# Kernel tuning notes

Hardware: AMD Instinct MI355X
Metric: run time of the kernel (lower is better)

The kernel has to match this reference:

```python
import jax, jax.numpy as jnp
import numpy as np

B, F, T, H, K = 512, 64, 64, 512, 4  # batch, in_feat, timesteps, hidden, num cells (air0,bed0,air1,bed1)


def setup_inputs() -> dict:
    key = jax.random.key(0)
    ks = jax.random.split(key, 10)
    s = 1.0 / np.sqrt(H)
    u = lambda k, shape: jax.random.uniform(k, shape, jnp.float32, -s, s)
    return {
        "data": jax.random.normal(ks[0], (B, F, T), jnp.float32),
        "init": jax.random.normal(ks[1], (B, H), jnp.float32),
        # stacked params for the 4 branches in order [air0, bed0, air1, bed1]
        "fc_in_W": u(ks[2], (K, H, F)),
        "fc_in_b": u(ks[3], (K, H)),
        "Wih": u(ks[4], (K, 3 * H, H)),   # torch GRUCell weight_ih, gate order r,z,n
        "Whh": u(ks[5], (K, 3 * H, H)),
        "bih": u(ks[6], (K, 3 * H)),
        "bhh": u(ks[7], (K, 3 * H)),
        "fc_out_W": u(ks[8], (2, H)),     # [air, bed] output heads (Linear(512,1))
        "fc_out_b": u(ks[9], (2,)),
    }


def reference(data, init, fc_in_W, fc_in_b, Wih, Whh, bih, bhh, fc_out_W, fc_out_b):
    # Input projections (Linear + ReLU; Dropout is identity in eval): [T, K, B, H]
    proj = jax.nn.relu(jnp.einsum('bft,kof->tkbo', data, fc_in_W) + fc_in_b[None, :, None, :])
    # branches 2,3 (air1, bed1) consume the sequence reversed (data[:, :, 63-i])
    x_seq = jnp.concatenate([proj[:, :2], proj[::-1, 2:]], axis=1)  # [T, K, B, H]

    h0 = jnp.broadcast_to(init[None], (K,) + init.shape)  # all 4 cells start from init

    def step(h, x):  # h, x: [K, B, H]
        gi = jnp.einsum('kbi,koi->kbo', x, Wih) + bih[:, None, :]
        gh = jnp.einsum('kbi,koi->kbo', h, Whh) + bhh[:, None, :]
        ir, iz, inn = jnp.split(gi, 3, axis=-1)
        hr, hz, hn = jnp.split(gh, 3, axis=-1)
        r = jax.nn.sigmoid(ir + hr)
        z = jax.nn.sigmoid(iz + hz)
        n = jnp.tanh(inn + r * hn)
        h_new = (1.0 - z) * n + z * h
        return h_new, h_new

    _, hs = jax.lax.scan(step, h0, x_seq)  # [T, K, B, H]

    # output i (1..64) combines fwd hidden[i] with bwd hidden[65-i] -> reverse bwd stack
    air = hs[:, 0] + hs[::-1, 2]  # [T, B, H]
    bed = hs[:, 1] + hs[::-1, 3]
    air_out = (jnp.einsum('tbh,h->tb', air, fc_out_W[0]) + fc_out_b[0]).T  # [B, T]
    bed_out = (jnp.einsum('tbh,h->tb', bed, fc_out_W[1]) + fc_out_b[1]).T
    return air_out, bed_out
```

## Files before the change

kernel.cpp:

```cpp
#include <hip/hip_runtime.h>
#include <hip/hip_bf16.h>

typedef __hip_bfloat16 bf16;
typedef __attribute__((ext_vector_type(8))) short short8;
typedef __attribute__((ext_vector_type(4))) float f32x4;

#define Hdim 512
#define Bdim 512
#define Tdim 64
#define Fdim 64
#define NC   4

__device__ __forceinline__ float sigmoidf_(float x){ return 1.f/(1.f + __expf(-x)); }
__device__ __forceinline__ float tanhf_(float x){
  float t = __expf(-2.f*fabsf(x));
  float r = (1.f - t)/(1.f + t);
  return copysignf(r, x);
}
__device__ __forceinline__ float bf2f_(short u){
  return __uint_as_float(((unsigned)(unsigned short)u) << 16);
}
__device__ __forceinline__ short f2bf_(float f){
  bf16 b = (bf16)f;
  return *(short*)&b;
}

__global__ __launch_bounds__(256) void pack_kernel(const float* __restrict__ src,
                                                   bf16* __restrict__ dst, int n){
  int idx = (blockIdx.x*256 + threadIdx.x)*4;
  if (idx < n){
    float4 v = *(const float4*)(src + idx);
    dst[idx+0] = (bf16)v.x;
    dst[idx+1] = (bf16)v.y;
    dst[idx+2] = (bf16)v.z;
    dst[idx+3] = (bf16)v.w;
  }
}

__global__ __launch_bounds__(256) void transpose_kernel(const float* __restrict__ data,
                                                        bf16* __restrict__ dataT){
  __shared__ bf16 tile[64*65];
  int b = blockIdx.x;
  int tid = threadIdx.x;
  for (int i = 0; i < 16; ++i){
    int idx = tid + i*256;
    int f = idx >> 6, t = idx & 63;
    tile[f*65 + t] = (bf16)data[(b*64 + f)*64 + t];
  }
  __syncthreads();
  for (int i = 0; i < 16; ++i){
    int idx = tid + i*256;
    int t = idx >> 6, f = idx & 63;
    dataT[(t*Bdim + b)*64 + f] = tile[f*65 + t];
  }
}

__global__ __launch_bounds__(256) void init_kernel(const float* __restrict__ init_h,
                            bf16* __restrict__ h_b1, unsigned* __restrict__ flags){
  int idx = blockIdx.x*256 + threadIdx.x;
  int k = idx >> 18;
  int rem = idx & 262143;
  int bg = rem >> 9;
  int o  = rem & 511;
  int dst = ((k*2 + (bg >> 8))*16 + (o >> 5))*8192 + (bg & 255)*32 + (o & 31);
  h_b1[dst] = (bf16)init_h[rem];
  if (idx < 512) flags[idx] = 0u;
}

__global__ __launch_bounds__(256) void proj_kernel(const bf16* __restrict__ dataT,
    const bf16* __restrict__ fc_in_W, const float* __restrict__ fc_in_b,
    bf16* __restrict__ x_seq){
  __shared__ short ldsA[64*72];
  __shared__ short ldsW[128*72];
  int blk = blockIdx.x;
  int s  = blk >> 7;
  int k  = (blk >> 5) & 3;
  int bt = (blk >> 2) & 7;
  int on = blk & 3;
  int tid = threadIdx.x;
  int lane = tid & 63, wid = tid >> 6;
  int quad = lane >> 4, l16 = lane & 15;
  int src_t = (k < 2) ? s : (Tdim - 1 - s);

  const short* Ag = (const short*)(dataT + (src_t*Bdim + bt*64)*Fdim);
  #pragma unroll
  for (int i = 0; i < 2; ++i){
    int c = tid + i*256; int r = c >> 3, off = c & 7;
    *(int4*)(&ldsA[r*72 + off*8]) = *(const int4*)(&Ag[r*64 + off*8]);
  }
  const short* Wg = (const short*)(fc_in_W + (k*Hdim + on*128)*Fdim);
  #pragma unroll
  for (int i = 0; i < 4; ++i){
    int c = tid + i*256; int r = c >> 3, off = c & 7;
    *(int4*)(&ldsW[r*72 + off*8]) = *(const int4*)(&Wg[r*64 + off*8]);
  }
  __syncthreads();

  f32x4 acc[2][4];
  #pragma unroll
  for (int nt=0; nt<2; ++nt)
    #pragma unroll
    for (int rb=0; rb<4; ++rb) acc[nt][rb] = (f32x4){0.f,0.f,0.f,0.f};

  #pragma unroll
  for (int kk = 0; kk < 2; ++kk){
    int io = kk*32 + quad*8;
    short8 a[4];
    #pragma unroll
    for (int rb=0; rb<4; ++rb) a[rb] = *(const short8*)(&ldsA[(rb*16+l16)*72 + io]);
    #pragma unroll
    for (int nt=0; nt<2; ++nt){
      short8 bw = *(const short8*)(&ldsW[(wid*32 + nt*16 + l16)*72 + io]);
      #pragma unroll
      for (int rb=0; rb<4; ++rb)
        acc[nt][rb] = __builtin_amdgcn_mfma_f32_16x16x32_bf16(a[rb], bw, acc[nt][rb], 0,0,0);
    }
  }

  #pragma unroll
  for (int nt=0; nt<2; ++nt){
    int o = on*128 + wid*32 + nt*16 + l16;
    float bias = fc_in_b[k*Hdim + o];
    #pragma unroll
    for (int rb=0; rb<4; ++rb){
      #pragma unroll
      for (int reg=0; reg<4; ++reg){
        int b = bt*64 + rb*16 + quad*4 + reg;
        float v = acc[nt][rb][reg] + bias;
        v = v > 0.f ? v : 0.f;
        x_seq[((size_t)(s*NC + k)*Bdim + b)*Hdim + o] = (bf16)v;
      }
    }
  }
}

__global__ __launch_bounds__(512) void rnn_kernel(
    const bf16* __restrict__ x_seq, const float* __restrict__ init_h,
    bf16* __restrict__ h_b0, bf16* __restrict__ h_b1,
    const float* __restrict__ Wih, const float* __restrict__ Whh,
    const float* __restrict__ bih, const float* __restrict__ bhh,
    const float* __restrict__ fc_out_W,
    bf16* __restrict__ gi, float* __restrict__ part,
    unsigned* __restrict__ flags, unsigned* __restrict__ xslot)
{
  __shared__ short wlds[3*2*16*512];
  __shared__ int sslot;

  int tid = threadIdx.x;
  int lane = tid & 63, wid = tid >> 6;
  int quad = lane >> 4, l16 = lane & 15;

  unsigned xcc;
  asm volatile("s_getreg_b32 %0, hwreg(HW_REG_XCC_ID)" : "=s"(xcc));
  xcc &= 7u;
  if (tid == 0)
    sslot = (int)__hip_atomic_fetch_add(&xslot[xcc*32], 1u,
                __ATOMIC_RELAXED, __HIP_MEMORY_SCOPE_WORKGROUP);
  __syncthreads();
  int grp = (int)xcc;
  int k   = grp >> 1;
  int bt  = grp & 1;
  int slot = sslot & 31;
  int producer = (slot < 16);
  int j    = slot & 15;
  int obase = j*32;
  int rot  = j;
  unsigned* gflags = flags + grp*32;

  const float* Wsrc = producer ? Wih : Whh;
  for (int i = tid; i < 3*2*16*64; i += 512){
    int plane = i >> 11;
    int rem   = i & 2047;
    int nt    = rem >> 10;
    int rem2  = rem & 1023;
    int kc    = rem2 >> 6;
    int ln    = rem2 & 63;
    int ll16  = ln & 15, lq = ln >> 4;
    const float* srcp = Wsrc +
        ((size_t)(k*3 + plane)*Hdim + obase + nt*16 + ll16)*Hdim + kc*32 + lq*8;
    float4 f0 = *(const float4*)srcp;
    float4 f1 = *(const float4*)(srcp + 4);
    short8 pk;
    pk[0]=f2bf_(f0.x); pk[1]=f2bf_(f0.y); pk[2]=f2bf_(f0.z); pk[3]=f2bf_(f0.w);
    pk[4]=f2bf_(f1.x); pk[5]=f2bf_(f1.y); pk[6]=f2bf_(f1.z); pk[7]=f2bf_(f1.w);
    *(int4*)(&wlds[i*8]) = *(int4*)&pk;
  }

  #define GEMM32X(ABASE) do {                                                   \
    const short* ap0_ = (ABASE) + (wid*32 + l16)*Hdim + quad*8;                 \
    const short* ap1_ = ap0_ + 16*Hdim;                                         \
    short8 ab_[4][2];                                                           \
    _Pragma("unroll")                                                           \
    for (int d=0; d<4; ++d){                                                    \
      int c_ = (d + rot) & 15;                                                  \
      ab_[d][0] = *(const short8*)(ap0_ + c_*32);                               \
      ab_[d][1] = *(const short8*)(ap1_ + c_*32);                               \
    }                                                                           \
    short8 bb_[2][6];                                                           \
    _Pragma("unroll")                                                           \
    for (int p=0; p<6; ++p)                                                     \
      bb_[0][p] = *(const short8*)(&wlds[((p*16 + rot)<<9) + (lane<<3)]);       \
    _Pragma("unroll")                                                           \
    for (int kc=0; kc<16; ++kc){                                                \
      short8 a0_ = ab_[kc&3][0], a1_ = ab_[kc&3][1];                            \
      if (kc < 12){                                                             \
        int c_ = (kc + 4 + rot) & 15;                                           \
        ab_[kc&3][0] = *(const short8*)(ap0_ + c_*32);                          \
        ab_[kc&3][1] = *(const short8*)(ap1_ + c_*32);                          \
      }                                                                         \
      if (kc < 15){                                                             \
        int c_ = (kc + 1 + rot) & 15;                                           \
        _Pragma("unroll")                                                       \
        for (int p=0; p<6; ++p)                                                 \
          bb_[(kc+1)&1][p] = *(const short8*)(&wlds[((p*16 + c_)<<9) + (lane<<3)]); \
      }                                                                         \
      _Pragma("unroll")                                                         \
      for (int g=0; g<3; ++g){                                                  \
        _Pragma("unroll")                                                       \
        for (int nt=0; nt<2; ++nt){                                             \
          short8 bw_ = bb_[kc&1][g*2+nt];                                       \
          acc[g][nt][0] = __builtin_amdgcn_mfma_f32_16x16x32_bf16(a0_, bw_, acc[g][nt][0], 0,0,0); \
          acc[g][nt][1] = __builtin_amdgcn_mfma_f32_16x16x32_bf16(a1_, bw_, acc[g][nt][1], 0,0,0); \
        }                                                                       \
      }                                                                         \
    }                                                                           \
  } while(0)

  #define GEMM32H(HCB) do {                                                     \
    const short* hp0_ = (HCB) + (wid*32 + l16)*32 + quad*8;                     \
    const short* hp1_ = hp0_ + 16*32;                                           \
    short8 ab_[4][2];                                                           \
    _Pragma("unroll")                                                           \
    for (int d=0; d<4; ++d){                                                    \
      int c_ = (d + rot) & 15;                                                  \
      ab_[d][0] = *(const short8*)(hp0_ + c_*8192);                             \
      ab_[d][1] = *(const short8*)(hp1_ + c_*8192);                             \
    }                                                                           \
    short8 bb_[2][6];                                                           \
    _Pragma("unroll")                                                           \
    for (int p=0; p<6; ++p)                                                     \
      bb_[0][p] = *(const short8*)(&wlds[((p*16 + rot)<<9) + (lane<<3)]);       \
    _Pragma("unroll")                                                           \
    for (int kc=0; kc<16; ++kc){                                                \
      short8 a0_ = ab_[kc&3][0], a1_ = ab_[kc&3][1];                            \
      if (kc < 12){                                                             \
        int c_ = (kc + 4 + rot) & 15;                                           \
        ab_[kc&3][0] = *(const short8*)(hp0_ + c_*8192);                        \
        ab_[kc&3][1] = *(const short8*)(hp1_ + c_*8192);                        \
      }                                                                         \
      if (kc < 15){                                                             \
        int c_ = (kc + 1 + rot) & 15;                                           \
        _Pragma("unroll")                                                       \
        for (int p=0; p<6; ++p)                                                 \
          bb_[(kc+1)&1][p] = *(const short8*)(&wlds[((p*16 + c_)<<9) + (lane<<3)]); \
      }                                                                         \
      _Pragma("unroll")                                                         \
      for (int g=0; g<3; ++g){                                                  \
        _Pragma("unroll")                                                       \
        for (int nt=0; nt<2; ++nt){                                             \
          short8 bw_ = bb_[kc&1][g*2+nt];                                       \
          acc[g][nt][0] = __builtin_amdgcn_mfma_f32_16x16x32_bf16(a0_, bw_, acc[g][nt][0], 0,0,0); \
          acc[g][nt][1] = __builtin_amdgcn_mfma_f32_16x16x32_bf16(a1_, bw_, acc[g][nt][1], 0,0,0); \
        }                                                                       \
      }                                                                         \
    }                                                                           \
  } while(0)

  if (producer){
    __syncthreads();
    for (int s = 0; s < 64; ++s){
      f32x4 acc[3][2][2];
      #pragma unroll
      for (int g=0; g<3; ++g)
        #pragma unroll
        for (int nt=0; nt<2; ++nt){
          acc[g][nt][0] = (f32x4){0.f,0.f,0.f,0.f};
          acc[g][nt][1] = (f32x4){0.f,0.f,0.f,0.f};
        }
      if (s >= 3){
        if (wid == 0){
          int g_ = 0;
          while (__hip_atomic_load(&gflags[16 + j], __ATOMIC_RELAXED,
                                   __HIP_MEMORY_SCOPE_AGENT) < (unsigned)(s - 2)){
            __builtin_amdgcn_s_sleep(1);
            if (++g_ > 4000000) break;
          }
        }
        __syncthreads();
      }
      const short* x_base = (const short*)(x_seq + ((size_t)(s*NC + k)*Bdim + bt*256)*Hdim);
      GEMM32X(x_base);
      bf16* gb = gi + ((size_t)(((s % 3)*8 + grp)*16 + j))*24576;
      #pragma unroll
      for (int g=0; g<3; ++g){
        #pragma unroll
        for (int nt=0; nt<2; ++nt){
          short8 pk;
          #pragma unroll
          for (int rb=0; rb<2; ++rb)
            #pragma unroll
            for (int reg=0; reg<4; ++reg)
              pk[rb*4+reg] = f2bf_(acc[g][nt][rb][reg]);
          *(int4*)(gb + ((g*2+nt)*512 + wid*64 + lane)*8) = *(int4*)&pk;
        }
      }
      __syncthreads();
      if (tid == 0)
        __hip_atomic_fetch_add(&gflags[j], 1u,
                               __ATOMIC_RELAXED, __HIP_MEMORY_SCOPE_AGENT);
    }
  } else {
    int o0 = obase + l16, o1 = o0 + 16;
    float br0  = bih[k*3*Hdim + o0] + bhh[k*3*Hdim + o0];
    float br1  = bih[k*3*Hdim + o1] + bhh[k*3*Hdim + o1];
    float bz0  = bih[k*3*Hdim + Hdim + o0] + bhh[k*3*Hdim + Hdim + o0];
    float bz1  = bih[k*3*Hdim + Hdim + o1] + bhh[k*3*Hdim + Hdim + o1];
    float bnx0 = bih[k*3*Hdim + 2*Hdim + o0];
    float bnx1 = bih[k*3*Hdim + 2*Hdim + o1];
    float bnh0 = bhh[k*3*Hdim + 2*Hdim + o0];
    float bnh1 = bhh[k*3*Hdim + 2*Hdim + o1];
    float wout0 = fc_out_W[(k & 1)*Hdim + o0];
    float wout1 = fc_out_W[(k & 1)*Hdim + o1];

    float hk[2][2][4];
    #pragma unroll
    for (int nt=0; nt<2; ++nt)
      #pragma unroll
      for (int rb=0; rb<2; ++rb)
        #pragma unroll
        for (int reg=0; reg<4; ++reg)
          hk[nt][rb][reg] =
            init_h[(bt*256 + wid*32 + rb*16 + quad*4 + reg)*Hdim + obase + nt*16 + l16];

    __syncthreads();

    const int hgrp = (k*2 + bt)*16;

    for (int s = 0; s < 64; ++s){
      const bf16* h_in  = (s & 1) ? h_b0 : h_b1;
      bf16*       h_out = (s & 1) ? h_b1 : h_b0;

      f32x4 acc[3][2][2];
      #pragma unroll
      for (int g=0; g<3; ++g)
        #pragma unroll
        for (int nt=0; nt<2; ++nt){
          acc[g][nt][0] = (f32x4){0.f,0.f,0.f,0.f};
          acc[g][nt][1] = (f32x4){0.f,0.f,0.f,0.f};
        }

      {
        if (wid == 0){
          int g_ = 0;
          for (;;){
            unsigned v_ = 0xFFFFFFFFu, thr_ = 0u;
            if (lane < 16){
              v_ = __hip_atomic_load(&gflags[16 + lane], __ATOMIC_RELAXED,
                                     __HIP_MEMORY_SCOPE_AGENT);
              thr_ = (unsigned)s;
            } else if (lane == 16){
              v_ = __hip_atomic_load(&gflags[j], __ATOMIC_RELAXED,
                                     __HIP_MEMORY_SCOPE_AGENT);
              thr_ = (unsigned)(s + 1);
            }
            if (__ballot(v_ >= thr_) == ~0ull) break;
            __builtin_amdgcn_s_sleep(1);
            if (++g_ > 4000000) break;
          }
        }
        __syncthreads();
      }

      const bf16* gb = gi + ((size_t)(((s % 3)*8 + grp)*16 + j))*24576;
      short8 gv[6];
      #pragma unroll
      for (int p=0; p<6; ++p){
        int4 t = *(const int4*)(gb + (p*512 + wid*64 + lane)*8);
        gv[p] = *(short8*)&t;
      }

      const short* h_cb = (const short*)h_in + (size_t)hgrp*8192;
      GEMM32H(h_cb);

      float hnv[2][2][4];
      bf16* hob = h_out + (size_t)(hgrp + j)*8192;
      #pragma unroll
      for (int rb = 0; rb < 2; ++rb){
        #pragma unroll
        for (int reg = 0; reg < 4; ++reg){
          int bl = wid*32 + rb*16 + quad*4 + reg;
          #pragma unroll
          for (int nt = 0; nt < 2; ++nt){
            float gir = bf2f_(gv[0*2+nt][rb*4+reg]);
            float giz = bf2f_(gv[1*2+nt][rb*4+reg]);
            float gin = bf2f_(gv[2*2+nt][rb*4+reg]);
            float br  = nt ? br1 : br0,  bz = nt ? bz1 : bz0;
            float bnx = nt ? bnx1 : bnx0, bnh = nt ? bnh1 : bnh0;
            float r = sigmoidf_(gir + acc[0][nt][rb][reg] + br);
            float z = sigmoidf_(giz + acc[1][nt][rb][reg] + bz);
            float n = tanhf_(gin + bnx + r*(acc[2][nt][rb][reg] + bnh));
            float hn = (1.f - z)*n + z*hk[nt][rb][reg];
            hk[nt][rb][reg] = hn;
            hnv[nt][rb][reg] = hn;
            hob[bl*32 + nt*16 + l16] = (bf16)hn;
          }
        }
      }

      __syncthreads();
      if (tid == 0)
        __hip_atomic_fetch_add(&gflags[16 + j], 1u,
                               __ATOMIC_RELAXED, __HIP_MEMORY_SCOPE_AGENT);

      int tmap = (k < 2) ? s : (Tdim - 1 - s);
      #pragma unroll
      for (int rb = 0; rb < 2; ++rb){
        #pragma unroll
        for (int reg = 0; reg < 4; ++reg){
          int bl = wid*32 + rb*16 + quad*4 + reg;
          float v = hnv[0][rb][reg]*wout0 + hnv[1][rb][reg]*wout1;
          v += __shfl_xor(v, 1, 64);
          v += __shfl_xor(v, 2, 64);
          v += __shfl_xor(v, 4, 64);
          v += __shfl_xor(v, 8, 64);
          if (l16 == 0)
            __builtin_nontemporal_store(v,
              &part[((size_t)(k*Tdim + tmap)*16 + j)*Bdim + bt*256 + bl]);
        }
      }
    }
  }
  #undef GEMM32X
  #undef GEMM32H
}

__global__ __launch_bounds__(256) void finalize_kernel(const float* __restrict__ part,
                                const float* __restrict__ fc_out_b, float* __restrict__ out){
  int idx = blockIdx.x*256 + threadIdx.x;
  int head = idx >> 15;
  int b = (idx >> 6) & 511;
  int t = idx & 63;
  float v = fc_out_b[head];
  #pragma unroll
  for (int kk = 0; kk < 2; ++kk){
    const float* p = part + (size_t)((head + kk*2)*Tdim + t)*16*Bdim + b;
    #pragma unroll
    for (int jj = 0; jj < 16; ++jj)
      v += p[jj*Bdim];
  }
  out[idx] = v;
}

extern "C" void kernel_launch(void* const* d_in, const int* in_sizes, int n_in,
                              void* d_out, int out_size, void* d_ws, size_t ws_size,
                              hipStream_t stream){
  (void)in_sizes; (void)n_in; (void)out_size; (void)ws_size;
  const float* data     = (const float*)d_in[0];
  const float* init_h   = (const float*)d_in[1];
  const float* fc_in_W  = (const float*)d_in[2];
  const float* fc_in_b  = (const float*)d_in[3];
  const float* Wih      = (const float*)d_in[4];
  const float* Whh      = (const float*)d_in[5];
  const float* bih      = (const float*)d_in[6];
  const float* bhh      = (const float*)d_in[7];
  const float* fc_out_W = (const float*)d_in[8];
  const float* fc_out_b = (const float*)d_in[9];
  float* out = (float*)d_out;

  char* ws = (char*)d_ws;
  bf16*  x_seq   = (bf16*)ws;
  bf16*  h_b0    = (bf16*)(ws + 134217728);
  bf16*  h_b1    = (bf16*)(ws + 136314880);
  bf16*  gi      = (bf16*)(ws + 138412032);
  bf16*  dataT   = (bf16*)(ws + 138412032);
  float* part    = (float*)(ws + 157286400);
  bf16*  fcW_bf  = (bf16*)(ws + 165675008);
  unsigned* flags= (unsigned*)(ws + 165937152);
  unsigned* xslot= (unsigned*)(ws + 165938176);

  const int nFW = NC*Hdim*Fdim;
  hipLaunchKernelGGL(pack_kernel, dim3(nFW/1024), dim3(256), 0, stream, fc_in_W, fcW_bf, nFW);
  hipLaunchKernelGGL(init_kernel, dim3(4096), dim3(256), 0, stream, init_h, h_b1, flags);
  hipLaunchKernelGGL(transpose_kernel, dim3(512), dim3(256), 0, stream, data, dataT);
  hipLaunchKernelGGL(proj_kernel, dim3(8192), dim3(256), 0, stream, dataT, fcW_bf, fc_in_b, x_seq);
  hipLaunchKernelGGL(rnn_kernel, dim3(256), dim3(512), 0, stream,
      x_seq, init_h, h_b0, h_b1, Wih, Whh, bih, bhh, fc_out_W, gi, part, flags, xslot);
  hipLaunchKernelGGL(finalize_kernel, dim3(256), dim3(256), 0, stream, part, fc_out_b, out);
}
```

Before: 740.7 us.

## Replace block-wide consumer barrier with per-wave, per-chunk readiness polling

```diff
diff --git a/kernel.cpp b/kernel.cpp
--- a/kernel.cpp
+++ b/kernel.cpp
@@ -23,6 +23,24 @@
 __device__ __forceinline__ short f2bf_(float f){
   bf16 b = (bf16)f;
   return *(short*)&b;
+}
+
+__device__ __forceinline__ unsigned rotl16_(unsigned m, int r){
+  return ((m << r) | (m >> ((16 - r) & 15))) & 0xFFFFu;
+}
+
+__device__ __forceinline__ unsigned poll_cons_(unsigned* cf, int lane,
+                                               unsigned need, unsigned thr){
+  int g_ = 0;
+  for (;;){
+    unsigned v = 0xFFFFFFFFu;
+    if (lane < 16)
+      v = __hip_atomic_load(&cf[lane], __ATOMIC_RELAXED, __HIP_MEMORY_SCOPE_AGENT);
+    unsigned m = (unsigned)__ballot(v >= thr) & 0xFFFFu;
+    if ((m & need) == need) return m;
+    __builtin_amdgcn_s_sleep(1);
+    if (++g_ > 4000000) return 0xFFFFu;
+  }
 }
 
 __global__ __launch_bounds__(256) void pack_kernel(const float* __restrict__ src,
@@ -226,46 +244,6 @@
     }                                                                           \
   } while(0)
 
-  #define GEMM32H(HCB) do {                                                     \
-    const short* hp0_ = (HCB) + (wid*32 + l16)*32 + quad*8;                     \
-    const short* hp1_ = hp0_ + 16*32;                                           \
-    short8 ab_[4][2];                                                           \
-    _Pragma("unroll")                                                           \
-    for (int d=0; d<4; ++d){                                                    \
-      int c_ = (d + rot) & 15;                                                  \
-      ab_[d][0] = *(const short8*)(hp0_ + c_*8192);                             \
-      ab_[d][1] = *(const short8*)(hp1_ + c_*8192);                             \
-    }                                                                           \
-    short8 bb_[2][6];                                                           \
-    _Pragma("unroll")                                                           \
-    for (int p=0; p<6; ++p)                                                     \
-      bb_[0][p] = *(const short8*)(&wlds[((p*16 + rot)<<9) + (lane<<3)]);       \
-    _Pragma("unroll")                                                           \
-    for (int kc=0; kc<16; ++kc){                                                \
-      short8 a0_ = ab_[kc&3][0], a1_ = ab_[kc&3][1];                            \
-      if (kc < 12){                                                             \
-        int c_ = (kc + 4 + rot) & 15;                                           \
-        ab_[kc&3][0] = *(const short8*)(hp0_ + c_*8192);                        \
-        ab_[kc&3][1] = *(const short8*)(hp1_ + c_*8192);                        \
-      }                                                                         \
-      if (kc < 15){                                                             \
-        int c_ = (kc + 1 + rot) & 15;                                           \
-        _Pragma("unroll")                                                       \
-        for (int p=0; p<6; ++p)                                                 \
-          bb_[(kc+1)&1][p] = *(const short8*)(&wlds[((p*16 + c_)<<9) + (lane<<3)]); \
-      }                                                                         \
-      _Pragma("unroll")                                                         \
-      for (int g=0; g<3; ++g){                                                  \
-        _Pragma("unroll")                                                       \
-        for (int nt=0; nt<2; ++nt){                                             \
-          short8 bw_ = bb_[kc&1][g*2+nt];                                       \
-          acc[g][nt][0] = __builtin_amdgcn_mfma_f32_16x16x32_bf16(a0_, bw_, acc[g][nt][0], 0,0,0); \
-          acc[g][nt][1] = __builtin_amdgcn_mfma_f32_16x16x32_bf16(a1_, bw_, acc[g][nt][1], 0,0,0); \
-        }                                                                       \
-      }                                                                         \
-    }                                                                           \
-  } while(0)
-
   if (producer){
     __syncthreads();
     for (int s = 0; s < 64; ++s){
@@ -335,6 +313,8 @@
     __syncthreads();
 
     const int hgrp = (k*2 + bt)*16;
+    unsigned* cf = gflags + 16;
+    const unsigned need0 = rotl16_(0x0Fu, rot);
 
     for (int s = 0; s < 64; ++s){
       const bf16* h_in  = (s & 1) ? h_b0 : h_b1;
@@ -349,26 +329,18 @@
           acc[g][nt][1] = (f32x4){0.f,0.f,0.f,0.f};
         }
 
+      short8 bb[2][6];
+      #pragma unroll
+      for (int p=0; p<6; ++p)
+        bb[0][p] = *(const short8*)(&wlds[((p*16 + rot)<<9) + (lane<<3)]);
+
       {
-        if (wid == 0){
-          int g_ = 0;
-          for (;;){
-            unsigned v_ = 0xFFFFFFFFu, thr_ = 0u;
-            if (lane < 16){
-              v_ = __hip_atomic_load(&gflags[16 + lane], __ATOMIC_RELAXED,
-                                     __HIP_MEMORY_SCOPE_AGENT);
-              thr_ = (unsigned)s;
-            } else if (lane == 16){
-              v_ = __hip_atomic_load(&gflags[j], __ATOMIC_RELAXED,
-                                     __HIP_MEMORY_SCOPE_AGENT);
-              thr_ = (unsigned)(s + 1);
-            }
-            if (__ballot(v_ >= thr_) == ~0ull) break;
-            __builtin_amdgcn_s_sleep(1);
-            if (++g_ > 4000000) break;
-          }
-        }
-        __syncthreads();
+        int g_ = 0;
+        while (__hip_atomic_load(&gflags[j], __ATOMIC_RELAXED,
+                                 __HIP_MEMORY_SCOPE_AGENT) < (unsigned)(s + 1)){
+          __builtin_amdgcn_s_sleep(1);
+          if (++g_ > 4000000) break;
+        }
       }
 
       const bf16* gb = gi + ((size_t)(((s % 3)*8 + grp)*16 + j))*24576;
@@ -379,8 +351,45 @@
         gv[p] = *(short8*)&t;
       }
 
+      unsigned rmask = poll_cons_(cf, lane, need0, (unsigned)s);
+
       const short* h_cb = (const short*)h_in + (size_t)hgrp*8192;
-      GEMM32H(h_cb);
+      const short* hp0 = h_cb + (wid*32 + l16)*32 + quad*8;
+      const short* hp1 = hp0 + 16*32;
+      short8 ab[4][2];
+      #pragma unroll
+      for (int d=0; d<4; ++d){
+        int c_ = (d + rot) & 15;
+        ab[d][0] = *(const short8*)(hp0 + c_*8192);
+        ab[d][1] = *(const short8*)(hp1 + c_*8192);
+      }
+      #pragma unroll
+      for (int kc=0; kc<16; ++kc){
+        short8 a0 = ab[kc&3][0], a1 = ab[kc&3][1];
+        if (kc < 12){
+          int cn = (kc + 4 + rot) & 15;
+          unsigned bit = 1u << cn;
+          if ((rmask & bit) == 0)
+            rmask |= poll_cons_(cf, lane, bit, (unsigned)s);
+          ab[kc&3][0] = *(const short8*)(hp0 + cn*8192);
+          ab[kc&3][1] = *(const short8*)(hp1 + cn*8192);
+        }
+        if (kc < 15){
+          int c_ = (kc + 1 + rot) & 15;
+          #pragma unroll
+          for (int p=0; p<6; ++p)
+            bb[(kc+1)&1][p] = *(const short8*)(&wlds[((p*16 + c_)<<9) + (lane<<3)]);
+        }
+        #pragma unroll
+        for (int g=0; g<3; ++g){
+          #pragma unroll
+          for (int nt=0; nt<2; ++nt){
+            short8 bw = bb[kc&1][g*2+nt];
+            acc[g][nt][0] = __builtin_amdgcn_mfma_f32_16x16x32_bf16(a0, bw, acc[g][nt][0], 0,0,0);
+            acc[g][nt][1] = __builtin_amdgcn_mfma_f32_16x16x32_bf16(a1, bw, acc[g][nt][1], 0,0,0);
+          }
+        }
+      }
 
       float hnv[2][2][4];
       bf16* hob = h_out + (size_t)(hgrp + j)*8192;
@@ -431,7 +440,6 @@
     }
   }
   #undef GEMM32X
-  #undef GEMM32H
 }
 
 __global__ __launch_bounds__(256) void finalize_kernel(const float* __restrict__ part,
```

Result: slower. 791.3 us (+6.8%).

## Merge producer/consumer RNN blocks into unified blocks computing both input and hidden GEMMs

Applied to the files above, without the earlier changes.

```diff
diff --git a/kernel.cpp b/kernel.cpp
--- a/kernel.cpp
+++ b/kernel.cpp
@@ -62,7 +62,7 @@
   int rem = idx & 262143;
   int bg = rem >> 9;
   int o  = rem & 511;
-  int dst = ((k*2 + (bg >> 8))*16 + (o >> 5))*8192 + (bg & 255)*32 + (o & 31);
+  int dst = ((k*2 + (bg >> 8))*32 + (o >> 4))*4096 + (bg & 255)*16 + (o & 15);
   h_b1[dst] = (bf16)init_h[rem];
   if (idx < 512) flags[idx] = 0u;
 }
@@ -134,16 +134,16 @@
   }
 }
 
-__global__ __launch_bounds__(512) void rnn_kernel(
+__global__ __launch_bounds__(512, 2) void rnn_kernel(
     const bf16* __restrict__ x_seq, const float* __restrict__ init_h,
     bf16* __restrict__ h_b0, bf16* __restrict__ h_b1,
     const float* __restrict__ Wih, const float* __restrict__ Whh,
     const float* __restrict__ bih, const float* __restrict__ bhh,
     const float* __restrict__ fc_out_W,
-    bf16* __restrict__ gi, float* __restrict__ part,
+    float* __restrict__ part,
     unsigned* __restrict__ flags, unsigned* __restrict__ xslot)
 {
-  __shared__ short wlds[3*2*16*512];
+  __shared__ short wlds[2*3*16*512];
   __shared__ int sslot;
 
   int tid = threadIdx.x;
@@ -160,24 +160,21 @@
   int grp = (int)xcc;
   int k   = grp >> 1;
   int bt  = grp & 1;
-  int slot = sslot & 31;
-  int producer = (slot < 16);
-  int j    = slot & 15;
-  int obase = j*32;
-  int rot  = j;
+  int j   = sslot & 31;
+  int rot = j & 15;
   unsigned* gflags = flags + grp*32;
 
-  const float* Wsrc = producer ? Wih : Whh;
-  for (int i = tid; i < 3*2*16*64; i += 512){
-    int plane = i >> 11;
-    int rem   = i & 2047;
-    int nt    = rem >> 10;
-    int rem2  = rem & 1023;
+  for (int i = tid; i < 6144; i += 512){
+    int side = (i >= 3072);
+    int i2   = i - side*3072;
+    int plane = i2 >> 10;
+    int rem2  = i2 & 1023;
     int kc    = rem2 >> 6;
     int ln    = rem2 & 63;
     int ll16  = ln & 15, lq = ln >> 4;
+    const float* Wsrc = side ? Whh : Wih;
     const float* srcp = Wsrc +
-        ((size_t)(k*3 + plane)*Hdim + obase + nt*16 + ll16)*Hdim + kc*32 + lq*8;
+        ((size_t)(k*3 + plane)*Hdim + j*16 + ll16)*Hdim + kc*32 + lq*8;
     float4 f0 = *(const float4*)srcp;
     float4 f1 = *(const float4*)(srcp + 4);
     short8 pk;
@@ -186,7 +183,29 @@
     *(int4*)(&wlds[i*8]) = *(int4*)&pk;
   }
 
-  #define GEMM32X(ABASE) do {                                                   \
+  int o0 = j*16 + l16;
+  float br  = bih[k*3*Hdim + o0] + bhh[k*3*Hdim + o0];
+  float bz  = bih[k*3*Hdim + Hdim + o0] + bhh[k*3*Hdim + Hdim + o0];
+  float bnx = bih[k*3*Hdim + 2*Hdim + o0];
+  float bnh = bhh[k*3*Hdim + 2*Hdim + o0];
+  float wout = fc_out_W[(k & 1)*Hdim + o0];
+
+  float hk[2][4];
+  #pragma unroll
+  for (int rb=0; rb<2; ++rb)
+    #pragma unroll
+    for (int reg=0; reg<4; ++reg)
+      hk[rb][reg] =
+        init_h[(bt*256 + wid*32 + rb*16 + quad*4 + reg)*Hdim + o0];
+
+  const size_t hgbase = (size_t)((k*2 + bt)*32) * 4096;
+
+  __syncthreads();
+
+  #define GEMM16X(ABASE, ACC) do {                                              \
+    _Pragma("unroll")                                                           \
+    for (int g=0; g<3; ++g){ ACC[g][0] = (f32x4){0.f,0.f,0.f,0.f};              \
+                             ACC[g][1] = (f32x4){0.f,0.f,0.f,0.f}; }            \
     const short* ap0_ = (ABASE) + (wid*32 + l16)*Hdim + quad*8;                 \
     const short* ap1_ = ap0_ + 16*Hdim;                                         \
     short8 ab_[4][2];                                                           \
@@ -196,10 +215,10 @@
       ab_[d][0] = *(const short8*)(ap0_ + c_*32);                               \
       ab_[d][1] = *(const short8*)(ap1_ + c_*32);                               \
     }                                                                           \
-    short8 bb_[2][6];                                                           \
-    _Pragma("unroll")                                                           \
-    for (int p=0; p<6; ++p)                                                     \
-      bb_[0][p] = *(const short8*)(&wlds[((p*16 + rot)<<9) + (lane<<3)]);       \
+    short8 bb_[2][3];                                                           \
+    _Pragma("unroll")                                                           \
+    for (int g=0; g<3; ++g)                                                     \
+      bb_[0][g] = *(const short8*)(&wlds[((g*16 + rot)<<9) + (lane<<3)]);       \
     _Pragma("unroll")                                                           \
     for (int kc=0; kc<16; ++kc){                                                \
       short8 a0_ = ab_[kc&3][0], a1_ = ab_[kc&3][1];                            \
@@ -211,24 +230,24 @@
       if (kc < 15){                                                             \
         int c_ = (kc + 1 + rot) & 15;                                           \
         _Pragma("unroll")                                                       \
-        for (int p=0; p<6; ++p)                                                 \
-          bb_[(kc+1)&1][p] = *(const short8*)(&wlds[((p*16 + c_)<<9) + (lane<<3)]); \
+        for (int g=0; g<3; ++g)                                                 \
+          bb_[(kc+1)&1][g] = *(const short8*)(&wlds[((g*16 + c_)<<9) + (lane<<3)]); \
       }                                                                         \
       _Pragma("unroll")                                                         \
       for (int g=0; g<3; ++g){                                                  \
-        _Pragma("unroll")                                                       \
-        for (int nt=0; nt<2; ++nt){                                             \
-          short8 bw_ = bb_[kc&1][g*2+nt];                                       \
-          acc[g][nt][0] = __builtin_amdgcn_mfma_f32_16x16x32_bf16(a0_, bw_, acc[g][nt][0], 0,0,0); \
-          acc[g][nt][1] = __builtin_amdgcn_mfma_f32_16x16x32_bf16(a1_, bw_, acc[g][nt][1], 0,0,0); \
-        }                                                                       \
+        short8 bw_ = bb_[kc&1][g];                                              \
+        ACC[g][0] = __builtin_amdgcn_mfma_f32_16x16x32_bf16(a0_, bw_, ACC[g][0], 0,0,0); \
+        ACC[g][1] = __builtin_amdgcn_mfma_f32_16x16x32_bf16(a1_, bw_, ACC[g][1], 0,0,0); \
       }                                                                         \
     }                                                                           \
   } while(0)
 
-  #define GEMM32H(HCB) do {                                                     \
-    const short* hp0_ = (HCB) + (wid*32 + l16)*32 + quad*8;                     \
-    const short* hp1_ = hp0_ + 16*32;                                           \
+  #define GEMM16H(HCB, ACC) do {                                                \
+    _Pragma("unroll")                                                           \
+    for (int g=0; g<3; ++g){ ACC[g][0] = (f32x4){0.f,0.f,0.f,0.f};              \
+                             ACC[g][1] = (f32x4){0.f,0.f,0.f,0.f}; }            \
+    const short* hp0_ = (HCB) + (quad>>1)*4096 + (wid*32 + l16)*16 + (quad&1)*8;\
+    const short* hp1_ = hp0_ + 256;                                             \
     short8 ab_[4][2];                                                           \
     _Pragma("unroll")                                                           \
     for (int d=0; d<4; ++d){                                                    \
@@ -236,10 +255,10 @@
       ab_[d][0] = *(const short8*)(hp0_ + c_*8192);                             \
       ab_[d][1] = *(const short8*)(hp1_ + c_*8192);                             \
     }                                                                           \
-    short8 bb_[2][6];                                                           \
-    _Pragma("unroll")                                                           \
-    for (int p=0; p<6; ++p)                                                     \
-      bb_[0][p] = *(const short8*)(&wlds[((p*16 + rot)<<9) + (lane<<3)]);       \
+    short8 bb_[2][3];                                                           \
+    _Pragma("unroll")                                                           \
+    for (int g=0; g<3; ++g)                                                     \
+      bb_[0][g] = *(const short8*)(&wlds[(((3+g)*16 + rot)<<9) + (lane<<3)]);   \
     _Pragma("unroll")                                                           \
     for (int kc=0; kc<16; ++kc){                                                \
       short8 a0_ = ab_[kc&3][0], a1_ = ab_[kc&3][1];                            \
@@ -251,187 +270,91 @@
       if (kc < 15){                                                             \
         int c_ = (kc + 1 + rot) & 15;                                           \
         _Pragma("unroll")                                                       \
-        for (int p=0; p<6; ++p)                                                 \
-          bb_[(kc+1)&1][p] = *(const short8*)(&wlds[((p*16 + c_)<<9) + (lane<<3)]); \
+        for (int g=0; g<3; ++g)                                                 \
+          bb_[(kc+1)&1][g] = *(const short8*)(&wlds[(((3+g)*16 + c_)<<9) + (lane<<3)]); \
       }                                                                         \
       _Pragma("unroll")                                                         \
       for (int g=0; g<3; ++g){                                                  \
-        _Pragma("unroll")                                                       \
-        for (int nt=0; nt<2; ++nt){                                             \
-          short8 bw_ = bb_[kc&1][g*2+nt];                                       \
-          acc[g][nt][0] = __builtin_amdgcn_mfma_f32_16x16x32_bf16(a0_, bw_, acc[g][nt][0], 0,0,0); \
-          acc[g][nt][1] = __builtin_amdgcn_mfma_f32_16x16x32_bf16(a1_, bw_, acc[g][nt][1], 0,0,0); \
+        short8 bw_ = bb_[kc&1][g];                                              \
+        ACC[g][0] = __builtin_amdgcn_mfma_f32_16x16x32_bf16(a0_, bw_, ACC[g][0], 0,0,0); \
+        ACC[g][1] = __builtin_amdgcn_mfma_f32_16x16x32_bf16(a1_, bw_, ACC[g][1], 0,0,0); \
+      }                                                                         \
+    }                                                                           \
+  } while(0)
+
+  #define STEP(S, GCUR, GNXT) do {                                              \
+    if ((S) < 63){                                                              \
+      const short* xb_ = (const short*)(x_seq +                                 \
+          ((size_t)(((S)+1)*NC + k)*Bdim + bt*256)*Hdim);                       \
+      GEMM16X(xb_, GNXT);                                                       \
+    }                                                                           \
+    if ((S) > 0){                                                               \
+      if (wid == 0){                                                            \
+        int g_ = 0;                                                             \
+        for (;;){                                                               \
+          unsigned v_ = 0xFFFFFFFFu;                                            \
+          if (lane < 32)                                                        \
+            v_ = __hip_atomic_load(&gflags[lane], __ATOMIC_RELAXED,             \
+                                   __HIP_MEMORY_SCOPE_AGENT);                   \
+          if (__ballot(v_ >= (unsigned)(S)) == ~0ull) break;                    \
+          __builtin_amdgcn_s_sleep(1);                                          \
+          if (++g_ > 4000000) break;                                            \
         }                                                                       \
       }                                                                         \
+      __syncthreads();                                                          \
+    }                                                                           \
+    const bf16* h_in_  = ((S) & 1) ? h_b0 : h_b1;                               \
+    bf16*       h_out_ = ((S) & 1) ? h_b1 : h_b0;                               \
+    f32x4 hacc_[3][2];                                                          \
+    GEMM16H((const short*)h_in_ + hgbase, hacc_);                               \
+    bf16* hob_ = h_out_ + hgbase + (size_t)j*4096;                              \
+    _Pragma("unroll")                                                           \
+    for (int rb = 0; rb < 2; ++rb){                                             \
+      _Pragma("unroll")                                                         \
+      for (int reg = 0; reg < 4; ++reg){                                        \
+        int bl_ = wid*32 + rb*16 + quad*4 + reg;                                \
+        float r_ = sigmoidf_(GCUR[0][rb][reg] + hacc_[0][rb][reg] + br);        \
+        float z_ = sigmoidf_(GCUR[1][rb][reg] + hacc_[1][rb][reg] + bz);        \
+        float n_ = tanhf_(GCUR[2][rb][reg] + bnx + r_*(hacc_[2][rb][reg] + bnh)); \
+        float hn_ = (1.f - z_)*n_ + z_*hk[rb][reg];                             \
+        hk[rb][reg] = hn_;                                                      \
+        hob_[bl_*16 + l16] = (bf16)hn_;                                         \
+      }                                                                         \
+    }                                                                           \
+    __syncthreads();                        \
+    if (tid == 0)                                                               \
+      __hip_atomic_fetch_add(&gflags[j], 1u,                                    \
+                             __ATOMIC_RELAXED, __HIP_MEMORY_SCOPE_AGENT);       \
+    int tmap_ = (k < 2) ? (S) : (Tdim - 1 - (S));                               \
+    _Pragma("unroll")                                                           \
+    for (int rb = 0; rb < 2; ++rb){                                             \
+      _Pragma("unroll")                                                         \
+      for (int reg = 0; reg < 4; ++reg){                                        \
+        int bl_ = wid*32 + rb*16 + quad*4 + reg;                                \
+        float v_ = hk[rb][reg]*wout;                                            \
+        v_ += __shfl_xor(v_, 1, 64);                                            \
+        v_ += __shfl_xor(v_, 2, 64);                                            \
+        v_ += __shfl_xor(v_, 4, 64);                                            \
+        v_ += __shfl_xor(v_, 8, 64);                                            \
+        if (l16 == 0)                                                           \
+          __builtin_nontemporal_store(v_,                                       \
+            &part[((size_t)(k*Tdim + tmap_)*Bdim + bt*256 + bl_)*32 + j]);      \
+      }                                                                         \
     }                                                                           \
   } while(0)
 
-  if (producer){
-    __syncthreads();
-    for (int s = 0; s < 64; ++s){
-      f32x4 acc[3][2][2];
-      #pragma unroll
-      for (int g=0; g<3; ++g)
-        #pragma unroll
-        for (int nt=0; nt<2; ++nt){
-          acc[g][nt][0] = (f32x4){0.f,0.f,0.f,0.f};
-          acc[g][nt][1] = (f32x4){0.f,0.f,0.f,0.f};
-        }
-      if (s >= 3){
-        if (wid == 0){
-          int g_ = 0;
-          while (__hip_atomic_load(&gflags[16 + j], __ATOMIC_RELAXED,
-                                   __HIP_MEMORY_SCOPE_AGENT) < (unsigned)(s - 2)){
-            __builtin_amdgcn_s_sleep(1);
-            if (++g_ > 4000000) break;
-          }
-        }
-        __syncthreads();
-      }
-      const short* x_base = (const short*)(x_seq + ((size_t)(s*NC + k)*Bdim + bt*256)*Hdim);
-      GEMM32X(x_base);
-      bf16* gb = gi + ((size_t)(((s % 3)*8 + grp)*16 + j))*24576;
-      #pragma unroll
-      for (int g=0; g<3; ++g){
-        #pragma unroll
-        for (int nt=0; nt<2; ++nt){
-          short8 pk;
-          #pragma unroll
-          for (int rb=0; rb<2; ++rb)
-            #pragma unroll
-            for (int reg=0; reg<4; ++reg)
-              pk[rb*4+reg] = f2bf_(acc[g][nt][rb][reg]);
-          *(int4*)(gb + ((g*2+nt)*512 + wid*64 + lane)*8) = *(int4*)&pk;
-        }
-      }
-      __syncthreads();
-      if (tid == 0)
-        __hip_atomic_fetch_add(&gflags[j], 1u,
-                               __ATOMIC_RELAXED, __HIP_MEMORY_SCOPE_AGENT);
-    }
-  } else {
-    int o0 = obase + l16, o1 = o0 + 16;
-    float br0  = bih[k*3*Hdim + o0] + bhh[k*3*Hdim + o0];
-    float br1  = bih[k*3*Hdim + o1] + bhh[k*3*Hdim + o1];
-    float bz0  = bih[k*3*Hdim + Hdim + o0] + bhh[k*3*Hdim + Hdim + o0];
-    float bz1  = bih[k*3*Hdim + Hdim + o1] + bhh[k*3*Hdim + Hdim + o1];
-    float bnx0 = bih[k*3*Hdim + 2*Hdim + o0];
-    float bnx1 = bih[k*3*Hdim + 2*Hdim + o1];
-    float bnh0 = bhh[k*3*Hdim + 2*Hdim + o0];
-    float bnh1 = bhh[k*3*Hdim + 2*Hdim + o1];
-    float wout0 = fc_out_W[(k & 1)*Hdim + o0];
-    float wout1 = fc_out_W[(k & 1)*Hdim + o1];
-
-    float hk[2][2][4];
-    #pragma unroll
-    for (int nt=0; nt<2; ++nt)
-      #pragma unroll
-      for (int rb=0; rb<2; ++rb)
-        #pragma unroll
-        for (int reg=0; reg<4; ++reg)
-          hk[nt][rb][reg] =
-            init_h[(bt*256 + wid*32 + rb*16 + quad*4 + reg)*Hdim + obase + nt*16 + l16];
-
-    __syncthreads();
-
-    const int hgrp = (k*2 + bt)*16;
-
-    for (int s = 0; s < 64; ++s){
-      const bf16* h_in  = (s & 1) ? h_b0 : h_b1;
-      bf16*       h_out = (s & 1) ? h_b1 : h_b0;
-
-      f32x4 acc[3][2][2];
-      #pragma unroll
-      for (int g=0; g<3; ++g)
-        #pragma unroll
-        for (int nt=0; nt<2; ++nt){
-          acc[g][nt][0] = (f32x4){0.f,0.f,0.f,0.f};
-          acc[g][nt][1] = (f32x4){0.f,0.f,0.f,0.f};
-        }
-
-      {
-        if (wid == 0){
-          int g_ = 0;
-          for (;;){
-            unsigned v_ = 0xFFFFFFFFu, thr_ = 0u;
-            if (lane < 16){
-              v_ = __hip_atomic_load(&gflags[16 + lane], __ATOMIC_RELAXED,
-                                     __HIP_MEMORY_SCOPE_AGENT);
-              thr_ = (unsigned)s;
-            } else if (lane == 16){
-              v_ = __hip_atomic_load(&gflags[j], __ATOMIC_RELAXED,
-                                     __HIP_MEMORY_SCOPE_AGENT);
-              thr_ = (unsigned)(s + 1);
-            }
-            if (__ballot(v_ >= thr_) == ~0ull) break;
-            __builtin_amdgcn_s_sleep(1);
-            if (++g_ > 4000000) break;
-          }
-        }
-        __syncthreads();
-      }
-
-      const bf16* gb = gi + ((size_t)(((s % 3)*8 + grp)*16 + j))*24576;
-      short8 gv[6];
-      #pragma unroll
-      for (int p=0; p<6; ++p){
-        int4 t = *(const int4*)(gb + (p*512 + wid*64 + lane)*8);
-        gv[p] = *(short8*)&t;
-      }
-
-      const short* h_cb = (const short*)h_in + (size_t)hgrp*8192;
-      GEMM32H(h_cb);
-
-      float hnv[2][2][4];
-      bf16* hob = h_out + (size_t)(hgrp + j)*8192;
-      #pragma unroll
-      for (int rb = 0; rb < 2; ++rb){
-        #pragma unroll
-        for (int reg = 0; reg < 4; ++reg){
-          int bl = wid*32 + rb*16 + quad*4 + reg;
-          #pragma unroll
-          for (int nt = 0; nt < 2; ++nt){
-            float gir = bf2f_(gv[0*2+nt][rb*4+reg]);
-            float giz = bf2f_(gv[1*2+nt][rb*4+reg]);
-            float gin = bf2f_(gv[2*2+nt][rb*4+reg]);
-            float br  = nt ? br1 : br0,  bz = nt ? bz1 : bz0;
-            float bnx = nt ? bnx1 : bnx0, bnh = nt ? bnh1 : bnh0;
-            float r = sigmoidf_(gir + acc[0][nt][rb][reg] + br);
-            float z = sigmoidf_(giz + acc[1][nt][rb][reg] + bz);
-            float n = tanhf_(gin + bnx + r*(acc[2][nt][rb][reg] + bnh));
-            float hn = (1.f - z)*n + z*hk[nt][rb][reg];
-            hk[nt][rb][reg] = hn;
-            hnv[nt][rb][reg] = hn;
-            hob[bl*32 + nt*16 + l16] = (bf16)hn;
-          }
-        }
-      }
-
-      __syncthreads();
-      if (tid == 0)
-        __hip_atomic_fetch_add(&gflags[16 + j], 1u,
-                               __ATOMIC_RELAXED, __HIP_MEMORY_SCOPE_AGENT);
-
-      int tmap = (k < 2) ? s : (Tdim - 1 - s);
-      #pragma unroll
-      for (int rb = 0; rb < 2; ++rb){
-        #pragma unroll
-        for (int reg = 0; reg < 4; ++reg){
-          int bl = wid*32 + rb*16 + quad*4 + reg;
-          float v = hnv[0][rb][reg]*wout0 + hnv[1][rb][reg]*wout1;
-          v += __shfl_xor(v, 1, 64);
-          v += __shfl_xor(v, 2, 64);
-          v += __shfl_xor(v, 4, 64);
-          v += __shfl_xor(v, 8, 64);
-          if (l16 == 0)
-            __builtin_nontemporal_store(v,
-              &part[((size_t)(k*Tdim + tmap)*16 + j)*Bdim + bt*256 + bl]);
-        }
-      }
-    }
-  }
-  #undef GEMM32X
-  #undef GEMM32H
+  f32x4 giA[3][2], giB[3][2];
+  {
+    const short* xb0 = (const short*)(x_seq + ((size_t)(k)*Bdim + bt*256)*Hdim);
+    GEMM16X(xb0, giA);
+  }
+  for (int sp = 0; sp < 32; ++sp){
+    STEP(2*sp,     giA, giB);
+    STEP(2*sp + 1, giB, giA);
+  }
+  #undef STEP
+  #undef GEMM16X
+  #undef GEMM16H
 }
 
 __global__ __launch_bounds__(256) void finalize_kernel(const float* __restrict__ part,
@@ -443,10 +366,13 @@
   float v = fc_out_b[head];
   #pragma unroll
   for (int kk = 0; kk < 2; ++kk){
-    const float* p = part + (size_t)((head + kk*2)*Tdim + t)*16*Bdim + b;
-    #pragma unroll
-    for (int jj = 0; jj < 16; ++jj)
-      v += p[jj*Bdim];
+    const float4* p = (const float4*)(part +
+        ((size_t)((head + kk*2)*Tdim + t)*Bdim + b)*32);
+    #pragma unroll
+    for (int jj = 0; jj < 8; ++jj){
+      float4 q = p[jj];
+      v += q.x + q.y + q.z + q.w;
+    }
   }
   out[idx] = v;
 }
@@ -471,9 +397,8 @@
   bf16*  x_seq   = (bf16*)ws;
   bf16*  h_b0    = (bf16*)(ws + 134217728);
   bf16*  h_b1    = (bf16*)(ws + 136314880);
-  bf16*  gi      = (bf16*)(ws + 138412032);
+  float* part    = (float*)(ws + 138412032);
   bf16*  dataT   = (bf16*)(ws + 138412032);
-  float* part    = (float*)(ws + 157286400);
   bf16*  fcW_bf  = (bf16*)(ws + 165675008);
   unsigned* flags= (unsigned*)(ws + 165937152);
   unsigned* xslot= (unsigned*)(ws + 165938176);
@@ -484,6 +409,6 @@
   hipLaunchKernelGGL(transpose_kernel, dim3(512), dim3(256), 0, stream, data, dataT);
   hipLaunchKernelGGL(proj_kernel, dim3(8192), dim3(256), 0, stream, dataT, fcW_bf, fc_in_b, x_seq);
   hipLaunchKernelGGL(rnn_kernel, dim3(256), dim3(512), 0, stream,
-      x_seq, init_h, h_b0, h_b1, Wih, Whh, bih, bhh, fc_out_W, gi, part, flags, xslot);
+      x_seq, init_h, h_b0, h_b1, Wih, Whh, bih, bhh, fc_out_W, part, flags, xslot);
   hipLaunchKernelGGL(finalize_kernel, dim3(256), dim3(256), 0, stream, part, fc_out_b, out);
 }
```

Result: slower. 936.1 us (+26.4%).
